# Kernel tuning notes

Hardware: AMD Instinct MI355X
Metric: run time of the kernel (lower is better)

## Reference

```python
import jax, jax.numpy as jnp
import numpy as np

D = 1024

def setup_inputs() -> dict:
    key = jax.random.key(0)
    ks = jax.random.split(key, 9)
    B, S = 4, 2048
    s = 1.0 / np.sqrt(D)
    return {
        "query": jax.random.normal(ks[0], (B, S, D), jnp.float32),
        "key": jax.random.normal(ks[1], (B, S, D), jnp.float32),
        "value": jax.random.normal(ks[2], (B, S, D), jnp.float32),
        "Wq": jax.random.normal(ks[3], (D, D), jnp.float32) * s,
        "bq": jax.random.normal(ks[4], (D,), jnp.float32) * 0.01,
        "Wk": jax.random.normal(ks[5], (D, D), jnp.float32) * s,
        "bk": jax.random.normal(ks[6], (D,), jnp.float32) * 0.01,
        "Wv": jax.random.normal(ks[7], (D, D), jnp.float32) * s,
        "bv": jax.random.normal(ks[8], (D,), jnp.float32) * 0.01,
    }

def reference(query, key, value, Wq, bq, Wk, bk, Wv, bv):
    scale = 1.0 / (query.shape[-1] ** 0.5)
    q = jnp.einsum('bsd,ed->bse', query, Wq) + bq  # nn.Linear: x @ W.T + b
    k = jnp.einsum('bsd,ed->bse', key, Wk) + bk
    v = jnp.einsum('bsd,ed->bse', value, Wv) + bv
    scores = jnp.einsum('bqd,bkd->bqk', q, k) * scale  # [B, Sq, Skv]
    w = jax.nn.softmax(scores, axis=-1)
    return jnp.einsum('bqk,bkd->bqd', w, v)
```

## Files before the change

kernel.cpp:

```cpp
#include <hip/hip_runtime.h>

typedef __bf16 bf16x8 __attribute__((ext_vector_type(8)));
typedef float f32x4 __attribute__((ext_vector_type(4)));
typedef unsigned short u16x8 __attribute__((ext_vector_type(8)));

__device__ inline unsigned short f2bf(float f) {
  union { float f; unsigned u; } a; a.f = f;
  return (unsigned short)((a.u + 0x7fffu + ((a.u >> 16) & 1u)) >> 16);
}
__device__ inline float bf2f(unsigned short h) {
  union { unsigned u; float f; } a; a.u = ((unsigned)h) << 16;
  return a.f;
}

__global__ __launch_bounds__(256) void cvtW(const float* __restrict__ Wq,
                                            const float* __restrict__ Wk,
                                            const float* __restrict__ Wv,
                                            unsigned short* __restrict__ Wb) {
  int i = blockIdx.x * 256 + threadIdx.x;
  int idx = i >> 18;
  int off = i & 262143;
  const float* s = (idx == 0) ? Wq : ((idx == 1) ? Wk : Wv);
  float4 v = ((const float4*)s)[off];
  ushort4 o;
  o.x = f2bf(v.x); o.y = f2bf(v.y); o.z = f2bf(v.z); o.w = f2bf(v.w);
  ((ushort4*)(Wb + idx * 1048576))[off] = o;
}

#define G2L(gp, lp) __builtin_amdgcn_global_load_lds( \
    (const __attribute__((address_space(1))) void*)(gp), \
    (__attribute__((address_space(3))) void*)(lp), 16, 0, 0)

#define MFMA_(d, a, b) d = __builtin_amdgcn_mfma_f32_16x16x32_bf16(a, b, d, 0, 0, 0)
#define SB0() __builtin_amdgcn_sched_barrier(0)
#define LGKM(n) do { asm volatile("s_waitcnt lgkmcnt(" #n ")" ::: "memory"); SB0(); } while (0)
#define VMC(n) do { asm volatile("s_waitcnt vmcnt(" #n ")" ::: "memory"); SB0(); } while (0)

struct PJ {
  const float* A0; const float* A1; const float* A2;
  const unsigned short* B;
  unsigned short* outQ; unsigned short* outK; unsigned short* outV;
  const float* biasQ; const float* biasK; const float* biasV;
};

__global__ __launch_bounds__(256) void gemmP(PJ p) {
  extern __shared__ char smem[];
  char* smA = smem;
  char* smB = smem + 32768;
  const int tid = threadIdx.x, lane = tid & 63, wid = tid >> 6;
  const int wm = wid >> 1, wn = wid & 1;

  int orig = blockIdx.x + 8 * (blockIdx.y + 64 * blockIdx.z);
  int wg = (orig & 7) * 192 + (orig >> 3);
  int bx = wg & 7; int t2 = wg >> 3; int by = t2 & 63; int z = t2 >> 6;
  const int m0 = by << 7, n0 = bx << 7;

  const float* Az = (z == 0) ? p.A0 : ((z == 1) ? p.A1 : p.A2);

  const char* srcA0 = (const char*)Az + ((long long)m0 + (tid >> 4)) * 4096
                    + ((tid & 15) << 4);
  const int trow = tid >> 3;
  const int cs = (((tid & 7) ^ (trow & 7)) << 4);
  const char* srcB = (const char*)(p.B + (long long)z * 1048576
                                   + (long long)(n0 + trow) * 1024) + cs;

  const int aRowB = (((wm << 6) + (lane & 15)) << 7);
  const int bRowB = (((wn << 6) + (lane & 15)) << 7);
  const int csw = (lane & 7) << 4;
  const int ck0 = (((lane >> 4) << 4)) ^ csw;
  const int ck1 = ((((lane >> 4) << 4)) | 64) ^ csw;

  f32x4 acc[4][4];
#pragma unroll
  for (int i = 0; i < 4; ++i)
#pragma unroll
    for (int j = 0; j < 4; ++j) acc[i][j] = (f32x4){0.f, 0.f, 0.f, 0.f};

  float4 areg[8];
  bf16x8 aLo[2][2], aHi[2][2], bLo[2][2], bHi[2][2];

  auto ldA = [&](int t) {
    const char* s = srcA0 + (long long)t * 256;
#pragma unroll
    for (int c = 0; c < 8; ++c)
      areg[c] = *(const float4*)(s + (long long)c * 65536);
  };
  auto wrA = [&](int t) {
    char* dA = smA + ((t & 1) << 14);
    const int g = (tid & 15) >> 1;
    const int hb = (tid & 1) << 3;
#pragma unroll
    for (int c = 0; c < 8; ++c) {
      const int rc = (c << 4) + (tid >> 4);
      float4 v = areg[c];
      ushort4 o;
      o.x = f2bf(v.x); o.y = f2bf(v.y); o.z = f2bf(v.z); o.w = f2bf(v.w);
      *(ushort4*)(dA + (rc << 7) + ((g ^ (rc & 7)) << 4) + hb) = o;
    }
  };
  auto stageB = [&](int t) {
    char* dB = smB + ((t & 1) << 14) + (tid << 4);
    const char* sB = srcB + (long long)t * 128;
#pragma unroll
    for (int c = 0; c < 4; ++c)
      G2L(sB + (long long)c * 65536, dB + (c << 12));
  };
  auto readAh = [&](int b, int half, bf16x8 (&dst)[2][2]) {
    const char* ra = smA + (b << 14) + aRowB + (half << 12);
#pragma unroll
    for (int mi = 0; mi < 2; ++mi) {
      dst[mi][0] = *(const bf16x8*)(ra + (mi << 11) + ck0);
      dst[mi][1] = *(const bf16x8*)(ra + (mi << 11) + ck1);
    }
  };
  auto readBh = [&](int b, int half, bf16x8 (&dst)[2][2]) {
    const char* rb = smB + (b << 14) + bRowB + (half << 12);
#pragma unroll
    for (int ni = 0; ni < 2; ++ni) {
      dst[ni][0] = *(const bf16x8*)(rb + (ni << 11) + ck0);
      dst[ni][1] = *(const bf16x8*)(rb + (ni << 11) + ck1);
    }
  };
  auto quad = [&](int qa, int qb, bf16x8 (&A)[2][2], bf16x8 (&B)[2][2]) {
    __builtin_amdgcn_s_setprio(1);
#pragma unroll
    for (int mi = 0; mi < 2; ++mi)
#pragma unroll
      for (int ni = 0; ni < 2; ++ni) {
        MFMA_(acc[qa * 2 + mi][qb * 2 + ni], A[mi][0], B[ni][0]);
        MFMA_(acc[qa * 2 + mi][qb * 2 + ni], A[mi][1], B[ni][1]);
      }
    __builtin_amdgcn_s_setprio(0);
  };

  ldA(0); stageB(0);
  VMC(4);
  wrA(0);
  VMC(0);
  LGKM(0);
  __builtin_amdgcn_s_barrier();
  readAh(0, 0, aLo); readBh(0, 0, bLo);
  SB0();

  const int NT = 16;
  for (int t = 0; t < NT; ++t) {
    const bool pf = (t + 1) < NT;
    if (pf) { ldA(t + 1); stageB(t + 1); }
    readAh(t & 1, 1, aHi);
    SB0();
    LGKM(4);
    quad(0, 0, aLo, bLo);
    readBh(t & 1, 1, bHi);
    SB0();
    LGKM(4);
    quad(1, 0, aHi, bLo);
    LGKM(0);
    quad(0, 1, aLo, bHi);
    quad(1, 1, aHi, bHi);
    if (pf) {
      VMC(4);
      wrA(t + 1);
      VMC(0);
    } else {
      VMC(0);
    }
    LGKM(0);
    __builtin_amdgcn_s_barrier();
    if (pf) { readAh((t + 1) & 1, 0, aLo); readBh((t + 1) & 1, 0, bLo); }
    SB0();
  }

  const int c0 = lane & 15, r0 = (lane >> 4) << 2;
  if (z < 2) {
    unsigned short* O = (z == 0) ? p.outQ : p.outK;
    const float* bias = (z == 0) ? p.biasQ : p.biasK;
#pragma unroll
    for (int mi = 0; mi < 4; ++mi) {
      const int grow = m0 + (wm << 6) + (mi << 4) + r0;
#pragma unroll
      for (int ni = 0; ni < 4; ++ni) {
        const int gcol = n0 + (wn << 6) + (ni << 4) + c0;
        const float bb = bias[gcol];
#pragma unroll
        for (int rr = 0; rr < 4; ++rr)
          O[(long long)(grow + rr) * 1024 + gcol] = f2bf(acc[mi][ni][rr] + bb);
      }
    }
  } else {
#pragma unroll
    for (int mi = 0; mi < 4; ++mi) {
      const int grow = m0 + (wm << 6) + (mi << 4) + r0;
      const int bb = grow >> 11, s = grow & 2047;
#pragma unroll
      for (int ni = 0; ni < 4; ++ni) {
        const int d = n0 + (wn << 6) + (ni << 4) + c0;
        const float ba = p.biasV[d];
        ushort4 pk;
        pk.x = f2bf(acc[mi][ni][0] + ba);
        pk.y = f2bf(acc[mi][ni][1] + ba);
        pk.z = f2bf(acc[mi][ni][2] + ba);
        pk.w = f2bf(acc[mi][ni][3] + ba);
        *(ushort4*)(p.outV + ((long long)bb << 21) + (long long)d * 2048 + s) = pk;
      }
    }
  }
}

#define EPI_SCALE 1
#define EPI_OUT 2

struct GP {
  const unsigned short* A;
  const unsigned short* B;
  unsigned short* C;
  long long batchA, batchB, batchC;
  int lda, ldb, ldc, K;
  float scale;
};

template<int BM, int BN, int WMW, int WNW, int EPI>
__global__ __launch_bounds__(512, 2) void gemm2(GP p) {
  constexpr int NWN = BN / WNW;
  constexpr int AMF = WMW / 16, BNF = WNW / 16;
  constexpr int AH = AMF / 2, BH = BNF / 2;
  constexpr int AF_N = AH * 2;
  constexpr int NBA = BM / 64, NBB = BN / 64;
  static_assert((BM / WMW) * NWN == 8, "8 waves");
  static_assert(BNF == 4, "lgkm immediates assume BNF==4");

  extern __shared__ char smem[];
  char* smA = smem;
  char* smB = smem + 2 * BM * 128;

  const int tid = threadIdx.x;
  const int lane = tid & 63;
  const int wid = tid >> 6;
  const int wm = wid / NWN, wn = wid % NWN;

  const int gx = gridDim.x, gy = gridDim.y;
  const int nwg = gx * gy * (int)gridDim.z;
  int orig = blockIdx.x + gx * (blockIdx.y + gy * blockIdx.z);
  int qq = nwg >> 3, rr_ = nwg & 7;
  int xcd = orig & 7, sl = orig >> 3;
  int wg = (xcd < rr_ ? xcd * (qq + 1) : rr_ * (qq + 1) + (xcd - rr_) * qq) + sl;
  int bx = wg % gx;
  int t2 = wg / gx;
  int by = t2 % gy;
  int z  = t2 / gy;

  const int m0 = by * BM, n0 = bx * BN;

  const long long lda2 = (long long)p.lda * 2;
  const long long ldb2 = (long long)p.ldb * 2;
  const char* Abase = (const char*)(p.A + (long long)z * p.batchA) + (long long)m0 * lda2;
  const char* Bbase = (const char*)(p.B + (long long)z * p.batchB) + (long long)n0 * ldb2;

  const int trow = tid >> 3;
  const int cs = (((tid & 7) ^ (trow & 7)) << 4);
  const char* srcA = Abase + (long long)trow * lda2 + cs;
  const char* srcB = Bbase + (long long)trow * ldb2 + cs;

  const int NT = p.K >> 6;

  const int aRowB = ((wm * WMW + (lane & 15)) << 7);
  const int bRowB = ((wn * WNW + (lane & 15)) << 7);
  const int csw = (lane & 7) << 4;
  const int ck0 = (((lane >> 4) << 4)) ^ csw;
  const int ck1 = ((((lane >> 4) << 4)) | 64) ^ csw;

  f32x4 acc[AMF][BNF];
#pragma unroll
  for (int i = 0; i < AMF; ++i)
#pragma unroll
    for (int j = 0; j < BNF; ++j) acc[i][j] = (f32x4){0.f, 0.f, 0.f, 0.f};

  bf16x8 aLo[AH][2], aHi[AH][2], bLo[BH][2], bHi[BH][2];

  auto stage = [&](int t) {
    char* dA = smA + (t & 1) * (BM * 128) + (tid << 4);
    char* dB = smB + (t & 1) * (BN * 128) + (tid << 4);
    const char* sA = srcA + (long long)t * 128;
    const char* sB = srcB + (long long)t * 128;
#pragma unroll
    for (int c = 0; c < NBA; ++c) G2L(sA + (long long)c * (lda2 << 6), dA + c * 8192);
#pragma unroll
    for (int c = 0; c < NBB; ++c) G2L(sB + (long long)c * (ldb2 << 6), dB + c * 8192);
  };
  auto readAh = [&](int t, int half, bf16x8 (&dst)[AH][2]) {
    const char* ra = smA + (t & 1) * (BM * 128) + aRowB + half * (AH * 2048);
#pragma unroll
    for (int mi = 0; mi < AH; ++mi) {
      dst[mi][0] = *(const bf16x8*)(ra + mi * 2048 + ck0);
      dst[mi][1] = *(const bf16x8*)(ra + mi * 2048 + ck1);
    }
  };
  auto readBh = [&](int t, int half, bf16x8 (&dst)[BH][2]) {
    const char* rb = smB + (t & 1) * (BN * 128) + bRowB + half * (BH * 2048);
#pragma unroll
    for (int ni = 0; ni < BH; ++ni) {
      dst[ni][0] = *(const bf16x8*)(rb + ni * 2048 + ck0);
      dst[ni][1] = *(const bf16x8*)(rb + ni * 2048 + ck1);
    }
  };
  auto quad = [&](int qa, int qb, bf16x8 (&A)[AH][2], bf16x8 (&B)[BH][2]) {
    __builtin_amdgcn_s_setprio(1);
#pragma unroll
    for (int mi = 0; mi < AH; ++mi)
#pragma unroll
      for (int ni = 0; ni < BH; ++ni) {
        MFMA_(acc[qa * AH + mi][qb * BH + ni], A[mi][0], B[ni][0]);
        MFMA_(acc[qa * AH + mi][qb * BH + ni], A[mi][1], B[ni][1]);
      }
    __builtin_amdgcn_s_setprio(0);
  };

  stage(0); stage(1);
  if constexpr (NBA + NBB == 8) VMC(8); else VMC(6);
  __builtin_amdgcn_s_barrier();
  readAh(0, 0, aLo); readBh(0, 0, bLo);
  SB0();

  for (int t = 0; t < NT; ++t) {
    readAh(t, 1, aHi);
    SB0();
    if constexpr (AF_N == 8) LGKM(8); else LGKM(4);
    quad(0, 0, aLo, bLo);
    readBh(t, 1, bHi);
    SB0();
    LGKM(4);
    quad(1, 0, aHi, bLo);
    LGKM(0);
    quad(0, 1, aLo, bHi);
    quad(1, 1, aHi, bHi);
    VMC(0);
    __builtin_amdgcn_s_barrier();
    if (t + 2 < NT) stage(t + 2);
    if (t + 1 < NT) { readAh(t + 1, 0, aLo); readBh(t + 1, 0, bLo); }
    SB0();
  }

  const int c0 = lane & 15;
  const int r0 = (lane >> 4) << 2;
  if constexpr (EPI == EPI_SCALE) {
    unsigned short* Cz = p.C + (long long)z * p.batchC;
#pragma unroll
    for (int mi = 0; mi < AMF; ++mi) {
      const int grow = m0 + wm * WMW + (mi << 4) + r0;
#pragma unroll
      for (int ni = 0; ni < BNF; ++ni) {
        const int gcol = n0 + wn * WNW + (ni << 4) + c0;
#pragma unroll
        for (int rr = 0; rr < 4; ++rr)
          Cz[(long long)(grow + rr) * p.ldc + gcol] = f2bf(acc[mi][ni][rr] * p.scale);
      }
    }
  } else {
    float* Cz = (float*)p.C + (long long)z * p.batchC;
#pragma unroll
    for (int mi = 0; mi < AMF; ++mi) {
      const int grow = m0 + wm * WMW + (mi << 4) + r0;
#pragma unroll
      for (int ni = 0; ni < BNF; ++ni) {
        const int gcol = n0 + wn * WNW + (ni << 4) + c0;
#pragma unroll
        for (int rr = 0; rr < 4; ++rr)
          Cz[(long long)(grow + rr) * p.ldc + gcol] = acc[mi][ni][rr] * p.scale;
      }
    }
  }
}

__global__ __launch_bounds__(256) void softmax_rows(unsigned short* __restrict__ S) {
  const size_t row = blockIdx.x;
  unsigned short* pp = S + row * 2048;
  const int t = threadIdx.x, lane = t & 63, wave = t >> 6;
  u16x8 h = ((const u16x8*)pp)[t];
  float x[8];
#pragma unroll
  for (int j = 0; j < 8; ++j) x[j] = bf2f(h[j]);
  float m = x[0];
#pragma unroll
  for (int j = 1; j < 8; ++j) m = fmaxf(m, x[j]);
#pragma unroll
  for (int off = 32; off >= 1; off >>= 1) m = fmaxf(m, __shfl_xor(m, off, 64));
  __shared__ float rmax[4], rsum[4];
  if (lane == 0) rmax[wave] = m;
  __syncthreads();
  m = fmaxf(fmaxf(rmax[0], rmax[1]), fmaxf(rmax[2], rmax[3]));
  float e[8], sum = 0.f;
#pragma unroll
  for (int j = 0; j < 8; ++j) { e[j] = __expf(x[j] - m); sum += e[j]; }
#pragma unroll
  for (int off = 32; off >= 1; off >>= 1) sum += __shfl_xor(sum, off, 64);
  if (lane == 0) rsum[wave] = sum;
  __syncthreads();
  sum = rsum[0] + rsum[1] + rsum[2] + rsum[3];
  const float inv = 1.f / sum;
  u16x8 o;
#pragma unroll
  for (int j = 0; j < 8; ++j) o[j] = f2bf(e[j] * inv);
  ((u16x8*)pp)[t] = o;
}

extern "C" void kernel_launch(void* const* d_in, const int* in_sizes, int n_in,
                              void* d_out, int out_size, void* d_ws, size_t ws_size,
                              hipStream_t stream) {
  const float* q  = (const float*)d_in[0];
  const float* k  = (const float*)d_in[1];
  const float* v  = (const float*)d_in[2];
  const float* Wq = (const float*)d_in[3];
  const float* bq = (const float*)d_in[4];
  const float* Wk = (const float*)d_in[5];
  const float* bk = (const float*)d_in[6];
  const float* Wv = (const float*)d_in[7];
  const float* bv = (const float*)d_in[8];

  unsigned short* S  = (unsigned short*)d_ws;
  unsigned short* Wb = S + 16777216;
  unsigned short* qb = Wb + 3145728;
  unsigned short* kb = qb + 8388608;
  unsigned short* vT = kb + 8388608;

  (void)hipFuncSetAttribute((const void*)gemmP,
      hipFuncAttributeMaxDynamicSharedMemorySize, 65536);
  (void)hipFuncSetAttribute((const void*)gemm2<256,256,128,64,EPI_SCALE>,
      hipFuncAttributeMaxDynamicSharedMemorySize, 131072);
  (void)hipFuncSetAttribute((const void*)gemm2<256,128,64,64,EPI_OUT>,
      hipFuncAttributeMaxDynamicSharedMemorySize, 98304);

  cvtW<<<3072, 256, 0, stream>>>(Wq, Wk, Wv, Wb);

  PJ pj{};
  pj.A0 = q; pj.A1 = k; pj.A2 = v;
  pj.B = Wb;
  pj.outQ = qb; pj.outK = kb; pj.outV = vT;
  pj.biasQ = bq; pj.biasK = bk; pj.biasV = bv;
  gemmP<<<dim3(8, 64, 3), 256, 65536, stream>>>(pj);

  GP gs{};
  gs.A = qb; gs.batchA = 2097152; gs.lda = 1024;
  gs.B = kb; gs.batchB = 2097152; gs.ldb = 1024;
  gs.C = S;  gs.batchC = 4194304; gs.ldc = 2048;
  gs.K = 1024; gs.scale = 0.03125f;
  gemm2<256,256,128,64,EPI_SCALE><<<dim3(8, 8, 4), 512, 131072, stream>>>(gs);

  softmax_rows<<<8192, 256, 0, stream>>>(S);

  GP gv{};
  gv.A = S;  gv.batchA = 4194304; gv.lda = 2048;
  gv.B = vT; gv.batchB = 2097152; gv.ldb = 2048;
  gv.C = (unsigned short*)d_out; gv.batchC = 2097152; gv.ldc = 1024;
  gv.K = 2048; gv.scale = 1.f;
  gemm2<256,128,64,64,EPI_OUT><<<dim3(8, 8, 4), 512, 98304, stream>>>(gv);
}
```

Baseline: 174.5 us.

## Deepen projection GEMM prefetch to two tiles ahead with triple-buffered B

The projection GEMM now issues global loads two K-tiles ahead. It uses two register sets for the fp32 A tile and three rotating LDS buffers for the B tile, which raises dynamic shared memory from 64KB to 80KB. The goal is to hide global load latency that the single-tile-ahead prefetch left exposed. The A conversion now uses a native __bf16 cast instead of the manual rounding helper. In exchange, register pressure rises from the extra float4[8] set and LDS use grows, which may reduce occupancy.

```diff
diff --git a/kernel.cpp b/kernel.cpp
--- a/kernel.cpp
+++ b/kernel.cpp
@@ -76,30 +76,31 @@
 #pragma unroll
     for (int j = 0; j < 4; ++j) acc[i][j] = (f32x4){0.f, 0.f, 0.f, 0.f};
 
-  float4 areg[8];
+  float4 aregA[8], aregB[8];
   bf16x8 aLo[2][2], aHi[2][2], bLo[2][2], bHi[2][2];
 
-  auto ldA = [&](int t) {
+  auto ldA = [&](int t, float4 (&ar)[8]) {
     const char* s = srcA0 + (long long)t * 256;
 #pragma unroll
     for (int c = 0; c < 8; ++c)
-      areg[c] = *(const float4*)(s + (long long)c * 65536);
-  };
-  auto wrA = [&](int t) {
+      ar[c] = *(const float4*)(s + (long long)c * 65536);
+  };
+  auto wrA = [&](int t, float4 (&ar)[8]) {
     char* dA = smA + ((t & 1) << 14);
     const int g = (tid & 15) >> 1;
     const int hb = (tid & 1) << 3;
 #pragma unroll
     for (int c = 0; c < 8; ++c) {
       const int rc = (c << 4) + (tid >> 4);
-      float4 v = areg[c];
-      ushort4 o;
-      o.x = f2bf(v.x); o.y = f2bf(v.y); o.z = f2bf(v.z); o.w = f2bf(v.w);
-      *(ushort4*)(dA + (rc << 7) + ((g ^ (rc & 7)) << 4) + hb) = o;
-    }
-  };
-  auto stageB = [&](int t) {
-    char* dB = smB + ((t & 1) << 14) + (tid << 4);
+      float4 v = ar[c];
+      union { __bf16 b[4]; ushort4 u; } o;
+      o.b[0] = (__bf16)v.x; o.b[1] = (__bf16)v.y;
+      o.b[2] = (__bf16)v.z; o.b[3] = (__bf16)v.w;
+      *(ushort4*)(dA + (rc << 7) + ((g ^ (rc & 7)) << 4) + hb) = o.u;
+    }
+  };
+  auto stageB = [&](int t, int b) {
+    char* dB = smB + (b << 14) + (tid << 4);
     const char* sB = srcB + (long long)t * 128;
 #pragma unroll
     for (int c = 0; c < 4; ++c)
@@ -133,42 +134,42 @@
     __builtin_amdgcn_s_setprio(0);
   };
 
-  ldA(0); stageB(0);
-  VMC(4);
-  wrA(0);
-  VMC(0);
+  const int NT = 16;
+  int b0 = 0, b1 = 1, b2 = 2;
+
+  ldA(0, aregA); stageB(0, 0);
+  ldA(1, aregB); stageB(1, 1);
+  VMC(12);
+  wrA(0, aregA);
   LGKM(0);
   __builtin_amdgcn_s_barrier();
   readAh(0, 0, aLo); readBh(0, 0, bLo);
   SB0();
 
-  const int NT = 16;
-  for (int t = 0; t < NT; ++t) {
-    const bool pf = (t + 1) < NT;
-    if (pf) { ldA(t + 1); stageB(t + 1); }
+  auto body = [&](int t, float4 (&arW)[8], float4 (&arL)[8]) {
+    const bool pf1 = (t + 1) < NT, pf2 = (t + 2) < NT;
+    if (pf2) { ldA(t + 2, arL); stageB(t + 2, b2); }
     readAh(t & 1, 1, aHi);
     SB0();
     LGKM(4);
     quad(0, 0, aLo, bLo);
-    readBh(t & 1, 1, bHi);
+    readBh(b0, 1, bHi);
     SB0();
     LGKM(4);
     quad(1, 0, aHi, bLo);
     LGKM(0);
     quad(0, 1, aLo, bHi);
     quad(1, 1, aHi, bHi);
-    if (pf) {
-      VMC(4);
-      wrA(t + 1);
-      VMC(0);
-    } else {
-      VMC(0);
-    }
+    if (pf2) { VMC(12); }
+    else     { VMC(0);  }
+    if (pf1) wrA(t + 1, arW);
     LGKM(0);
     __builtin_amdgcn_s_barrier();
-    if (pf) { readAh((t + 1) & 1, 0, aLo); readBh((t + 1) & 1, 0, bLo); }
-    SB0();
-  }
+    if (pf1) { readAh((t + 1) & 1, 0, aLo); readBh(b1, 0, bLo); }
+    SB0();
+    int tmp = b0; b0 = b1; b1 = b2; b2 = tmp;
+  };
+  for (int t = 0; t < NT; t += 2) { body(t, aregB, aregA); body(t + 1, aregA, aregB); }
 
   const int c0 = lane & 15, r0 = (lane >> 4) << 2;
   if (z < 2) {
@@ -422,7 +423,7 @@
   unsigned short* vT = kb + 8388608;
 
   (void)hipFuncSetAttribute((const void*)gemmP,
-      hipFuncAttributeMaxDynamicSharedMemorySize, 65536);
+      hipFuncAttributeMaxDynamicSharedMemorySize, 81920);
   (void)hipFuncSetAttribute((const void*)gemm2<256,256,128,64,EPI_SCALE>,
       hipFuncAttributeMaxDynamicSharedMemorySize, 131072);
   (void)hipFuncSetAttribute((const void*)gemm2<256,128,64,64,EPI_OUT>,
@@ -435,7 +436,7 @@
   pj.B = Wb;
   pj.outQ = qb; pj.outK = kb; pj.outV = vT;
   pj.biasQ = bq; pj.biasK = bk; pj.biasV = bv;
-  gemmP<<<dim3(8, 64, 3), 256, 65536, stream>>>(pj);
+  gemmP<<<dim3(8, 64, 3), 256, 81920, stream>>>(pj);
 
   GP gs{};
   gs.A = qb; gs.batchA = 2097152; gs.lda = 1024;
```

After: 166.9 us. 1.05x faster.
